# Performance work log

Measured on AMD Instinct MI355X. Metric: run time of the kernel, lower is better.

The kernel has to match this reference:

```python
import jax, jax.numpy as jnp
import numpy as np
from jax import lax

B, C, H, W = 32, 684, 16, 64
HID, A, CK, K = 256, 512, 512, 11


def setup_inputs() -> dict:
    key = jax.random.key(0)
    ks = jax.random.split(key, 12)
    s = 0.02
    return {
        "cnn_features": jax.random.normal(ks[0], (B, C, H, W), jnp.float32),
        "hidden": jax.random.normal(ks[1], (B, HID), jnp.float32),
        "alpha_sum": jax.random.uniform(ks[2], (B, 1, H, W), jnp.float32),
        "image_mask": jnp.ones((B, 1, H, W), jnp.float32),
        # hidden_weight: Linear(HID -> A)
        "Wh": jax.random.normal(ks[3], (A, HID), jnp.float32) * s,
        "bh": jnp.zeros((A,), jnp.float32),
        # encoder_feature_conv: Conv2d(C -> A, 1x1) == pointwise linear
        "Wec": jax.random.normal(ks[4], (A, C), jnp.float32) * s,
        "bec": jnp.zeros((A,), jnp.float32),
        # attention_conv: Conv2d(1 -> CK, 11x11, pad 5, no bias)
        "Wac": jax.random.normal(ks[5], (CK, 1, K, K), jnp.float32) * s,
        # attention_weight: Linear(CK -> A, no bias)
        "Waw": jax.random.normal(ks[6], (A, CK), jnp.float32) * s,
        # alpha_convert: Linear(A -> 1)
        "Wv": jax.random.normal(ks[7], (1, A), jnp.float32) * s,
        "bv": jnp.zeros((1,), jnp.float32),
    }


def reference(cnn_features, hidden, alpha_sum, image_mask,
              Wh, bh, Wec, bec, Wac, Waw, Wv, bv):
    # query = hidden_weight(hidden): [B, A]
    query = hidden @ Wh.T + bh
    # attention_conv(alpha_sum): [B, CK, H, W]
    ast = lax.conv_general_dilated(
        alpha_sum, Wac, window_strides=(1, 1),
        padding=[(K // 2, K // 2), (K // 2, K // 2)],
        dimension_numbers=("NCHW", "OIHW", "NCHW"))
    # attention_weight on permuted conv output: [B, H, W, A]
    coverage_alpha = jnp.einsum("bkhw,ak->bhwa", ast, Waw)
    # encoder_feature_conv (1x1 conv == pointwise linear): [B, H, W, A]
    cnn_trans = jnp.einsum("bchw,ac->bhwa", cnn_features, Wec) + bec
    # additive attention score
    alpha_score = jnp.tanh(query[:, None, None, :] + coverage_alpha + cnn_trans)
    # alpha_convert -> scalar energy per position: [B, H, W]
    energy = jnp.einsum("bhwa,a->bhw", alpha_score, Wv[0]) + bv[0]
    energy = energy - energy.max()  # global max-subtract as in original
    energy_exp = jnp.exp(energy) * image_mask[:, 0]
    denom = energy_exp.sum(axis=(-1, -2))[:, None, None] + 1e-10
    alpha = energy_exp / denom  # [B, H, W]
    alpha_sum_new = alpha[:, None, :, :] + alpha_sum  # [B, 1, H, W]
    # context: weighted spatial sum over features -> [B, C]
    context_vector = jnp.einsum("bhw,bchw->bc", alpha, cnn_features)
    return (context_vector, alpha, alpha_sum_new)
```

## Files before the change

### kernel.cpp

```cpp
#include <hip/hip_runtime.h>
#include <hip/hip_bf16.h>
#include <math.h>

#define Bn   32
#define Cn   684
#define Hn   16
#define Wn   64
#define HWn  1024
#define HIDn 256
#define An   512
#define KKn  121
#define CREAL 805
#define CPAD 832
#define NSTEP 26
#define NBLK 256

#define OUT_ALPHA 21888
#define OUT_ASUM  (21888 + 32768)

typedef short short8 __attribute__((ext_vector_type(8)));
typedef float floatx4 __attribute__((ext_vector_type(4)));

__device__ __forceinline__ unsigned short f2bf(float f) {
    union { float f; unsigned int i; } v; v.f = f;
    unsigned int i = v.i;
    return (unsigned short)((i + 0x7fffu + ((i >> 16) & 1u)) >> 16);
}
__device__ __forceinline__ unsigned int cvt2(float lo, float hi) {
    __hip_bfloat162 h = __float22bfloat162_rn(float2{lo, hi});
    union { __hip_bfloat162 h; unsigned int u; } cv; cv.h = h;
    return cv.u;
}

__device__ __forceinline__ size_t bfr_idx(int n, int k) {
    return ((((size_t)(n >> 4) * 26 + (k >> 5)) * 64
             + ((k >> 3) & 3) * 16 + (n & 15)) * 8) + (k & 7);
}

__global__ __launch_bounds__(256) void k_prep(
    const float* __restrict__ hidden,
    const float* __restrict__ Wh,
    const float* __restrict__ bh,
    const float* __restrict__ bec,
    const float* __restrict__ Wec,
    const float* __restrict__ Wac,
    const float* __restrict__ Waw,
    float* __restrict__ query,
    unsigned short* __restrict__ Bfr,
    float* __restrict__ energy)
{
    __shared__ float sbuf[512];
    const int blk = blockIdx.x, t = threadIdx.x;
    if (blk < 512) {
        const int a = blk;
        sbuf[t]       = Waw[(size_t)a * 512 + t];
        sbuf[t + 256] = Waw[(size_t)a * 512 + t + 256];
        __syncthreads();
        for (int cp = t; cp < Cn; cp += 256)
            Bfr[bfr_idx(a, cp)] = f2bf(Wec[(size_t)a * Cn + cp]);
        if (t < KKn) {
            float s = 0.f;
            #pragma unroll 8
            for (int k = 0; k < 512; ++k)
                s = fmaf(sbuf[k], Wac[k * KKn + t], s);
            Bfr[bfr_idx(a, Cn + t)] = f2bf(s);
        }
        for (int cp = CREAL + t; cp < CPAD; cp += 256)
            Bfr[bfr_idx(a, cp)] = 0;
    } else if (blk < 544) {
        const int b = blk - 512;
        sbuf[t] = (t < HIDn) ? hidden[b * HIDn + t] : 0.f;
        __syncthreads();
        for (int a = t; a < An; a += 256) {
            const float4* wp = (const float4*)(Wh + (size_t)a * HIDn);
            float s = bh[a] + bec[a];
            #pragma unroll 8
            for (int i = 0; i < HIDn / 4; ++i) {
                float4 w = wp[i];
                s = fmaf(sbuf[4 * i],     w.x, s);
                s = fmaf(sbuf[4 * i + 1], w.y, s);
                s = fmaf(sbuf[4 * i + 2], w.z, s);
                s = fmaf(sbuf[4 * i + 3], w.w, s);
            }
            query[b * An + a] = s;
        }
    } else {
        const int b = blk - 544;
        #pragma unroll
        for (int i = 0; i < 4; ++i)
            energy[b * HWn + i * 256 + t] = 0.f;
    }
}

__global__ __launch_bounds__(512, 4) void k_energy(
    const float* __restrict__ X,
    const float* __restrict__ asum,
    const float* __restrict__ Wv,
    const float* __restrict__ query,
    const unsigned short* __restrict__ Bfr,
    float* __restrict__ energy)
{
    __shared__ __align__(16) unsigned short As[2][64 * 40];
    __shared__ float plane[878];
    __shared__ int   lut[148];
    __shared__ float qs[NBLK];
    __shared__ float wvs[NBLK];
    __shared__ float red[8][64];

    const int t = threadIdx.x;
    const int d = blockIdx.x;
    const int nh  = (d >> 3) & 1;
    const int pid = (d >> 4) * 8 + (d & 7);
    const int hh = pid & 15, b = pid >> 4;
    const int w = t >> 6, lane = t & 63;
    const int q = lane >> 4, r = lane & 15;
    const int nbase = nh * NBLK;
    const int mA = lane;

    const float* Xb = X + (size_t)b * Cn * HWn + hh * Wn;
    const unsigned short* Bp = Bfr + (size_t)(nh * 16 + w * 2) * 26 * 512;

    for (int i = t; i < 878; i += 512) {
        float v = 0.f;
        if (i < 814) {
            int di = i / 74, cc = i - di * 74;
            int h2 = hh + di - 5, w2 = cc - 5;
            if (h2 >= 0 && h2 < Hn && w2 >= 0 && w2 < Wn)
                v = asum[b * HWn + h2 * Wn + w2];
        }
        plane[i] = v;
    }
    if (t < 148) {
        int off = 814;
        if (t < 121) { int di = t / 11; off = di * 74 + (t - di * 11); }
        lut[t] = off;
    }
    if (t < NBLK) {
        qs[t]  = query[b * An + nbase + t];
        wvs[t] = Wv[nbase + t];
    }
    {
        const float* xp = Xb + (size_t)(w * 4) * HWn + mA;
        float v0 = xp[0];
        float v1 = xp[(size_t)1 * HWn];
        float v2 = xp[(size_t)2 * HWn];
        float v3 = xp[(size_t)3 * HWn];
        *(uint2*)&As[0][mA * 40 + w * 4] = make_uint2(cvt2(v0, v1), cvt2(v2, v3));
    }

    short8 bfA[2], bfB[2];
    float vaA[4], vaB[4];

    #pragma unroll
    for (int nf = 0; nf < 2; ++nf)
        bfA[nf] = *(const short8*)(Bp + ((size_t)(nf * 26)) * 512 + lane * 8);
    {
        const float* xp = Xb + (size_t)(32 + w * 4) * HWn + mA;
        vaA[0] = xp[0];
        vaA[1] = xp[(size_t)1 * HWn];
        vaA[2] = xp[(size_t)2 * HWn];
        vaA[3] = xp[(size_t)3 * HWn];
    }
    __syncthreads();

    floatx4 acc[4][2];
    #pragma unroll
    for (int mf = 0; mf < 4; ++mf)
        #pragma unroll
        for (int nf = 0; nf < 2; ++nf)
            acc[mf][nf] = (floatx4){0.f, 0.f, 0.f, 0.f};

#define ISSUE_BF(DST, CC) {                                                   \
    const int cb_ = (CC) <= 25 ? (CC) : 25;                                   \
    _Pragma("unroll")                                                         \
    for (int nf = 0; nf < 2; ++nf)                                            \
        DST[nf] = *(const short8*)(Bp + ((size_t)(nf * 26 + cb_)) * 512       \
                                      + lane * 8);                            \
    }

#define ISSUE_VA(DST, CC) {                                                   \
    const int cc_ = (CC) <= 25 ? (CC) : 25;                                   \
    const int c0_ = cc_ * 32 + w * 4;                                         \
    _Pragma("unroll")                                                         \
    for (int j = 0; j < 4; ++j) {                                             \
        const int row = c0_ + j;                                              \
        if (row < Cn) DST[j] = Xb[(size_t)row * HWn + mA];                    \
        else          DST[j] = plane[lut[row - Cn] + mA];                     \
    } }

#define READA(CUR) {                                                          \
    _Pragma("unroll")                                                         \
    for (int mf = 0; mf < 4; ++mf)                                            \
        af[mf] = *(const short8*)&As[CUR][(mf * 16 + r) * 40 + q * 8];        \
    }

#define MFMA8(BF) {                                                           \
    _Pragma("unroll")                                                         \
    for (int mf = 0; mf < 4; ++mf)                                            \
        _Pragma("unroll")                                                     \
        for (int nf = 0; nf < 2; ++nf)                                        \
            acc[mf][nf] = __builtin_amdgcn_mfma_f32_16x16x32_bf16(            \
                af[mf], BF[nf], acc[mf][nf], 0, 0, 0);                        \
    }

#define WRITEA(CUR, SRC) {                                                    \
    *(uint2*)&As[CUR][mA * 40 + w * 4] =                                      \
        make_uint2(cvt2(SRC[0], SRC[1]), cvt2(SRC[2], SRC[3]));               \
    }

#define LOOP_BARRIER() {                                                      \
    asm volatile("s_waitcnt lgkmcnt(0)" ::: "memory");                        \
    __builtin_amdgcn_sched_barrier(0);                                        \
    __builtin_amdgcn_s_barrier();                                             \
    __builtin_amdgcn_sched_barrier(0);                                        \
    }

    short8 af[4];
    for (int ch = 0; ch < NSTEP; ch += 2) {
        READA(0);
        ISSUE_BF(bfB, ch + 1);
        ISSUE_VA(vaB, ch + 2);
        MFMA8(bfA);
        WRITEA(1, vaA);
        LOOP_BARRIER();

        READA(1);
        ISSUE_BF(bfA, ch + 2);
        ISSUE_VA(vaA, ch + 3);
        MFMA8(bfB);
        if (ch + 2 < NSTEP) WRITEA(0, vaB);
        LOOP_BARRIER();
    }

#undef ISSUE_BF
#undef ISSUE_VA
#undef READA
#undef MFMA8
#undef WRITEA
#undef LOOP_BARRIER

    float ep[16];
    #pragma unroll
    for (int i = 0; i < 16; ++i) ep[i] = 0.f;
    #pragma unroll
    for (int nf = 0; nf < 2; ++nf) {
        int nl = w * 32 + nf * 16 + r;
        float qv = qs[nl], wv = wvs[nl];
        #pragma unroll
        for (int mf = 0; mf < 4; ++mf)
            #pragma unroll
            for (int rg = 0; rg < 4; ++rg) {
                float x = acc[mf][nf][rg] + qv;
                float e2 = __expf(2.f * x);
                float th = 1.f - 2.f * __builtin_amdgcn_rcpf(e2 + 1.f);
                ep[mf * 4 + rg] += wv * th;
            }
    }
    #pragma unroll
    for (int i = 0; i < 16; ++i) {
        #pragma unroll
        for (int msk = 1; msk <= 8; msk <<= 1)
            ep[i] += __shfl_xor(ep[i], msk, 64);
    }
    if (r == 0) {
        #pragma unroll
        for (int mf = 0; mf < 4; ++mf)
            #pragma unroll
            for (int rg = 0; rg < 4; ++rg)
                red[w][mf * 16 + q * 4 + rg] = ep[mf * 4 + rg];
    }
    __syncthreads();
    if (t < 64) {
        float s = 0.f;
        #pragma unroll
        for (int ww = 0; ww < 8; ++ww) s += red[ww][t];
        atomicAdd(&energy[b * HWn + hh * Wn + t], s);
    }
}

__global__ __launch_bounds__(256) void k_softmax(
    const float* __restrict__ mask,
    const float* __restrict__ asum,
    float* __restrict__ energy,
    float* __restrict__ out)
{
    __shared__ float rsm[8];
    const int b = blockIdx.x;
    const int t = threadIdx.x, lane = t & 63, wid = t >> 6;

    float e[4], ex[4];
    #pragma unroll
    for (int i = 0; i < 4; ++i) e[i] = energy[b * HWn + i * 256 + t];
    float m = fmaxf(fmaxf(e[0], e[1]), fmaxf(e[2], e[3]));
    for (int off = 32; off >= 1; off >>= 1) m = fmaxf(m, __shfl_down(m, off, 64));
    if (lane == 0) rsm[wid] = m;
    __syncthreads();
    if (t == 0)
        rsm[4] = fmaxf(fmaxf(rsm[0], rsm[1]), fmaxf(rsm[2], rsm[3]));
    __syncthreads();
    const float M = rsm[4];
    float s = 0.f;
    #pragma unroll
    for (int i = 0; i < 4; ++i) {
        ex[i] = expf(e[i] - M) * mask[b * HWn + i * 256 + t];
        s += ex[i];
    }
    for (int off = 32; off >= 1; off >>= 1) s += __shfl_down(s, off, 64);
    __syncthreads();
    if (lane == 0) rsm[wid] = s;
    __syncthreads();
    if (t == 0) rsm[5] = rsm[0] + rsm[1] + rsm[2] + rsm[3] + 1e-10f;
    __syncthreads();
    const float denom = rsm[5];
    #pragma unroll
    for (int i = 0; i < 4; ++i) {
        int p = i * 256 + t;
        float a = ex[i] / denom;
        energy[b * HWn + p] = a;
        out[OUT_ALPHA + b * HWn + p] = a;
        out[OUT_ASUM  + b * HWn + p] = a + asum[b * HWn + p];
    }
}

__global__ __launch_bounds__(256) void k_ctx(
    const float* __restrict__ X,
    const float* __restrict__ alpha,
    float* __restrict__ out)
{
    __shared__ float al[1024];
    const int bx = blockIdx.x, b = blockIdx.y;
    const int t = threadIdx.x, lane = t & 63, wid = t >> 6;

    #pragma unroll
    for (int i = 0; i < 4; ++i) al[i * 256 + t] = alpha[b * HWn + i * 256 + t];
    __syncthreads();

    const int c = bx * 4 + wid;
    const float* xp = X + ((size_t)(b * Cn + c)) * HWn;
    float s2 = 0.f;
    #pragma unroll
    for (int i = 0; i < 4; ++i) {
        int off = i * 256 + lane * 4;
        float4 x = *(const float4*)(xp + off);
        float4 a = *(const float4*)(al + off);
        s2 = fmaf(a.x, x.x, s2);
        s2 = fmaf(a.y, x.y, s2);
        s2 = fmaf(a.z, x.z, s2);
        s2 = fmaf(a.w, x.w, s2);
    }
    for (int off = 32; off >= 1; off >>= 1) s2 += __shfl_down(s2, off, 64);
    if (lane == 0) out[b * Cn + c] = s2;
}

extern "C" void kernel_launch(void* const* d_in, const int* in_sizes, int n_in,
                              void* d_out, int out_size, void* d_ws, size_t ws_size,
                              hipStream_t stream)
{
    const float* X      = (const float*)d_in[0];
    const float* hidden = (const float*)d_in[1];
    const float* asum   = (const float*)d_in[2];
    const float* mask   = (const float*)d_in[3];
    const float* Wh     = (const float*)d_in[4];
    const float* bh     = (const float*)d_in[5];
    const float* Wec    = (const float*)d_in[6];
    const float* bec    = (const float*)d_in[7];
    const float* Wac    = (const float*)d_in[8];
    const float* Waw    = (const float*)d_in[9];
    const float* Wv     = (const float*)d_in[10];
    (void)in_sizes; (void)n_in; (void)out_size; (void)ws_size;

    float* out = (float*)d_out;
    float* ws = (float*)d_ws;
    float* query  = ws;
    float* energy = ws + 16384;
    unsigned short* Bfr = (unsigned short*)(ws + 16384 + 32768);

    k_prep    <<<dim3(576),      dim3(256), 0, stream>>>(hidden, Wh, bh, bec,
                                                         Wec, Wac, Waw, query, Bfr, energy);
    k_energy  <<<dim3(1024),     dim3(512), 0, stream>>>(X, asum, Wv, query, Bfr, energy);
    k_softmax <<<dim3(32),       dim3(256), 0, stream>>>(mask, asum, energy, out);
    k_ctx     <<<dim3(171, 32),  dim3(256), 0, stream>>>(X, energy, out);
}
```

Before: 240.3 us.

## Compute full attention dim per block to halve X reads and drop atomics

Each k_energy block now covers all 512 attention columns (four N-fragments per wave) instead of splitting N across two blocks. Each X tile is therefore loaded and converted once rather than twice, and energy is written directly instead of atomically accumulated. The main loop becomes single-stepped with a separate tail for the coverage-plane rows, and the MFMA section is wrapped in s_setprio. The cost is more accumulator registers and half as many blocks (512), which may reduce occupancy and latency hiding.

After: 231.8 us. 1.04x faster.

```diff
diff --git a/kernel.cpp b/kernel.cpp
--- a/kernel.cpp
+++ b/kernel.cpp
@@ -13,7 +13,6 @@
 #define CREAL 805
 #define CPAD 832
 #define NSTEP 26
-#define NBLK 256
 
 #define OUT_ALPHA 21888
 #define OUT_ASUM  (21888 + 32768)
@@ -92,6 +91,13 @@
     }
 }
 
+__device__ __forceinline__ float fetchU(const float* __restrict__ Xb,
+                                        const float* plane, const int* lut,
+                                        int m, int row) {
+    if (row < Cn) return Xb[(size_t)row * HWn + m];
+    return plane[lut[row - Cn] + m];
+}
+
 __global__ __launch_bounds__(512, 4) void k_energy(
     const float* __restrict__ X,
     const float* __restrict__ asum,
@@ -103,22 +109,19 @@
     __shared__ __align__(16) unsigned short As[2][64 * 40];
     __shared__ float plane[878];
     __shared__ int   lut[148];
-    __shared__ float qs[NBLK];
-    __shared__ float wvs[NBLK];
+    __shared__ float qs[512];
+    __shared__ float wvs[512];
     __shared__ float red[8][64];
 
     const int t = threadIdx.x;
     const int d = blockIdx.x;
-    const int nh  = (d >> 3) & 1;
-    const int pid = (d >> 4) * 8 + (d & 7);
-    const int hh = pid & 15, b = pid >> 4;
+    const int hh = d & 15, b = d >> 4;
     const int w = t >> 6, lane = t & 63;
     const int q = lane >> 4, r = lane & 15;
-    const int nbase = nh * NBLK;
     const int mA = lane;
 
     const float* Xb = X + (size_t)b * Cn * HWn + hh * Wn;
-    const unsigned short* Bp = Bfr + (size_t)(nh * 16 + w * 2) * 26 * 512;
+    const unsigned short* Bp = Bfr + (size_t)(w * 4) * 26 * 512;
 
     for (int i = t; i < 878; i += 512) {
         float v = 0.f;
@@ -135,10 +138,8 @@
         if (t < 121) { int di = t / 11; off = di * 74 + (t - di * 11); }
         lut[t] = off;
     }
-    if (t < NBLK) {
-        qs[t]  = query[b * An + nbase + t];
-        wvs[t] = Wv[nbase + t];
-    }
+    qs[t]  = query[b * An + t];
+    wvs[t] = Wv[t];
     {
         const float* xp = Xb + (size_t)(w * 4) * HWn + mA;
         float v0 = xp[0];
@@ -148,45 +149,27 @@
         *(uint2*)&As[0][mA * 40 + w * 4] = make_uint2(cvt2(v0, v1), cvt2(v2, v3));
     }
 
-    short8 bfA[2], bfB[2];
-    float vaA[4], vaB[4];
-
-    #pragma unroll
-    for (int nf = 0; nf < 2; ++nf)
-        bfA[nf] = *(const short8*)(Bp + ((size_t)(nf * 26)) * 512 + lane * 8);
+    short8 bf[4], af[4];
+    float va[4];
+
     {
         const float* xp = Xb + (size_t)(32 + w * 4) * HWn + mA;
-        vaA[0] = xp[0];
-        vaA[1] = xp[(size_t)1 * HWn];
-        vaA[2] = xp[(size_t)2 * HWn];
-        vaA[3] = xp[(size_t)3 * HWn];
-    }
-    __syncthreads();
-
-    floatx4 acc[4][2];
+        va[0] = xp[0];
+        va[1] = xp[(size_t)1 * HWn];
+        va[2] = xp[(size_t)2 * HWn];
+        va[3] = xp[(size_t)3 * HWn];
+    }
+    #pragma unroll
+    for (int nf = 0; nf < 4; ++nf)
+        bf[nf] = *(const short8*)(Bp + ((size_t)(nf * 26)) * 512 + lane * 8);
+    __syncthreads();
+
+    floatx4 acc[4][4];
     #pragma unroll
     for (int mf = 0; mf < 4; ++mf)
         #pragma unroll
-        for (int nf = 0; nf < 2; ++nf)
+        for (int nf = 0; nf < 4; ++nf)
             acc[mf][nf] = (floatx4){0.f, 0.f, 0.f, 0.f};
-
-#define ISSUE_BF(DST, CC) {                                                   \
-    const int cb_ = (CC) <= 25 ? (CC) : 25;                                   \
-    _Pragma("unroll")                                                         \
-    for (int nf = 0; nf < 2; ++nf)                                            \
-        DST[nf] = *(const short8*)(Bp + ((size_t)(nf * 26 + cb_)) * 512       \
-                                      + lane * 8);                            \
-    }
-
-#define ISSUE_VA(DST, CC) {                                                   \
-    const int cc_ = (CC) <= 25 ? (CC) : 25;                                   \
-    const int c0_ = cc_ * 32 + w * 4;                                         \
-    _Pragma("unroll")                                                         \
-    for (int j = 0; j < 4; ++j) {                                             \
-        const int row = c0_ + j;                                              \
-        if (row < Cn) DST[j] = Xb[(size_t)row * HWn + mA];                    \
-        else          DST[j] = plane[lut[row - Cn] + mA];                     \
-    } }
 
 #define READA(CUR) {                                                          \
     _Pragma("unroll")                                                         \
@@ -194,18 +177,27 @@
         af[mf] = *(const short8*)&As[CUR][(mf * 16 + r) * 40 + q * 8];        \
     }
 
-#define MFMA8(BF) {                                                           \
+#define WRITEA(CUR) {                                                         \
+    *(uint2*)&As[CUR][mA * 40 + w * 4] =                                      \
+        make_uint2(cvt2(va[0], va[1]), cvt2(va[2], va[3]));                   \
+    }
+
+#define MFMA16() {                                                            \
+    __builtin_amdgcn_s_setprio(1);                                            \
     _Pragma("unroll")                                                         \
     for (int mf = 0; mf < 4; ++mf)                                            \
         _Pragma("unroll")                                                     \
-        for (int nf = 0; nf < 2; ++nf)                                        \
+        for (int nf = 0; nf < 4; ++nf)                                        \
             acc[mf][nf] = __builtin_amdgcn_mfma_f32_16x16x32_bf16(            \
-                af[mf], BF[nf], acc[mf][nf], 0, 0, 0);                        \
-    }
-
-#define WRITEA(CUR, SRC) {                                                    \
-    *(uint2*)&As[CUR][mA * 40 + w * 4] =                                      \
-        make_uint2(cvt2(SRC[0], SRC[1]), cvt2(SRC[2], SRC[3]));               \
+                af[mf], bf[nf], acc[mf][nf], 0, 0, 0);                        \
+    __builtin_amdgcn_s_setprio(0);                                            \
+    }
+
+#define ISSUE_BF(CC) {                                                        \
+    _Pragma("unroll")                                                         \
+    for (int nf = 0; nf < 4; ++nf)                                            \
+        bf[nf] = *(const short8*)(Bp + ((size_t)(nf * 26 + (CC))) * 512       \
+                                     + lane * 8);                             \
     }
 
 #define LOOP_BARRIER() {                                                      \
@@ -215,36 +207,50 @@
     __builtin_amdgcn_sched_barrier(0);                                        \
     }
 
-    short8 af[4];
-    for (int ch = 0; ch < NSTEP; ch += 2) {
-        READA(0);
-        ISSUE_BF(bfB, ch + 1);
-        ISSUE_VA(vaB, ch + 2);
-        MFMA8(bfA);
-        WRITEA(1, vaA);
+    const float* xva = Xb + (size_t)(64 + w * 4) * HWn + mA;
+    const size_t chstep = (size_t)32 * HWn;
+
+    for (int ch = 0; ch < 18; ++ch) {
+        const int cur = ch & 1;
+        READA(cur);
+        WRITEA(cur ^ 1);
+        MFMA16();
+        va[0] = xva[0];
+        va[1] = xva[(size_t)1 * HWn];
+        va[2] = xva[(size_t)2 * HWn];
+        va[3] = xva[(size_t)3 * HWn];
+        xva += chstep;
+        ISSUE_BF(ch + 1);
         LOOP_BARRIER();
-
-        READA(1);
-        ISSUE_BF(bfA, ch + 2);
-        ISSUE_VA(vaA, ch + 3);
-        MFMA8(bfB);
-        if (ch + 2 < NSTEP) WRITEA(0, vaB);
+    }
+
+    for (int ch = 18; ch < NSTEP; ++ch) {
+        const int cur = ch & 1;
+        READA(cur);
+        if (ch < NSTEP - 1) WRITEA(cur ^ 1);
+        MFMA16();
+        const int cva = (ch + 2 <= 25) ? (ch + 2) : 25;
+        const int c0 = cva * 32 + w * 4;
+        #pragma unroll
+        for (int j = 0; j < 4; ++j)
+            va[j] = fetchU(Xb, plane, lut, mA, c0 + j);
+        const int cbf = (ch + 1 <= 25) ? (ch + 1) : 25;
+        ISSUE_BF(cbf);
         LOOP_BARRIER();
     }
 
+#undef READA
+#undef WRITEA
+#undef MFMA16
 #undef ISSUE_BF
-#undef ISSUE_VA
-#undef READA
-#undef MFMA8
-#undef WRITEA
 #undef LOOP_BARRIER
 
     float ep[16];
     #pragma unroll
     for (int i = 0; i < 16; ++i) ep[i] = 0.f;
     #pragma unroll
-    for (int nf = 0; nf < 2; ++nf) {
-        int nl = w * 32 + nf * 16 + r;
+    for (int nf = 0; nf < 4; ++nf) {
+        int nl = w * 64 + nf * 16 + r;
         float qv = qs[nl], wv = wvs[nl];
         #pragma unroll
         for (int mf = 0; mf < 4; ++mf)
@@ -274,7 +280,7 @@
         float s = 0.f;
         #pragma unroll
         for (int ww = 0; ww < 8; ++ww) s += red[ww][t];
-        atomicAdd(&energy[b * HWn + hh * Wn + t], s);
+        energy[b * HWn + hh * Wn + t] = s;
     }
 }
 
@@ -377,7 +383,7 @@
 
     k_prep    <<<dim3(576),      dim3(256), 0, stream>>>(hidden, Wh, bh, bec,
                                                          Wec, Wac, Waw, query, Bfr, energy);
-    k_energy  <<<dim3(1024),     dim3(512), 0, stream>>>(X, asum, Wv, query, Bfr, energy);
+    k_energy  <<<dim3(512),      dim3(512), 0, stream>>>(X, asum, Wv, query, Bfr, energy);
     k_softmax <<<dim3(32),       dim3(256), 0, stream>>>(mask, asum, energy, out);
     k_ctx     <<<dim3(171, 32),  dim3(256), 0, stream>>>(X, energy, out);
 }
```
